# Optimization experiments

Measured on AMD Instinct MI355X. Metric: run time of the kernel, lower is better.

The kernel has to match this reference:

```python
import jax, jax.numpy as jnp
import numpy as np

D_MODEL = 1024
HEADS = 16
D_K = D_MODEL // HEADS
D_FF = 4096
EPS = 1e-6


def setup_inputs() -> dict:
    key = jax.random.key(0)
    ks = jax.random.split(key, 16)
    s = 1.0 / np.sqrt(D_MODEL)
    inp = {
        'x': jax.random.normal(ks[0], (4, 2048, D_MODEL), dtype=jnp.float32),
        'Wq': jax.random.normal(ks[1], (D_MODEL, D_MODEL), dtype=jnp.float32) * s,
        'bq': jnp.zeros((D_MODEL,), jnp.float32),
        'Wk': jax.random.normal(ks[2], (D_MODEL, D_MODEL), dtype=jnp.float32) * s,
        'bk': jnp.zeros((D_MODEL,), jnp.float32),
        'Wv': jax.random.normal(ks[3], (D_MODEL, D_MODEL), dtype=jnp.float32) * s,
        'bv': jnp.zeros((D_MODEL,), jnp.float32),
        'Wo': jax.random.normal(ks[4], (D_MODEL, D_MODEL), dtype=jnp.float32) * s,
        'bo': jnp.zeros((D_MODEL,), jnp.float32),
        'alpha1': jnp.ones((D_MODEL,), jnp.float32),
        'bias1': jnp.zeros((D_MODEL,), jnp.float32),
        'alpha2': jnp.ones((D_MODEL,), jnp.float32),
        'bias2': jnp.zeros((D_MODEL,), jnp.float32),
        'W1': jax.random.normal(ks[5], (D_MODEL, D_FF), dtype=jnp.float32) * s,
        'b1': jnp.zeros((D_FF,), jnp.float32),
        'W2': jax.random.normal(ks[6], (D_FF, D_MODEL), dtype=jnp.float32) * (1.0 / np.sqrt(D_FF)),
        'b2': jnp.zeros((D_MODEL,), jnp.float32),
    }
    return inp


def _residual_norm(x, residual, alpha, bias):
    # x = x + residual; norm with mean and UNBIASED std (torch x.std default),
    # eps added to std (not variance), affine alpha/bias. Dropout = identity (eval).
    s = x + residual
    mean = jnp.mean(s, axis=-1, keepdims=True)
    std = jnp.std(s, axis=-1, keepdims=True, ddof=1)
    return alpha * (s - mean) / (std + EPS) + bias


def _forward(x, Wq, bq, Wk, bk, Wv, bv, Wo, bo, alpha1, bias1, alpha2, bias2, W1, b1, W2, b2):
    B, S, D = x.shape
    # QKV projections and head split: (B, H, S, d_k)
    def split_heads(t):
        return t.reshape(B, S, HEADS, D_K).transpose(0, 2, 1, 3)
    Q = split_heads(x @ Wq + bq)
    K = split_heads(x @ Wk + bk)
    V = split_heads(x @ Wv + bv)
    # scaled dot-product attention (no mask, no dropout in eval)
    scores = jnp.einsum('bhqd,bhkd->bhqk', Q, K) / np.sqrt(D_K)
    weights = jax.nn.softmax(scores, axis=-1)
    attn = jnp.einsum('bhqk,bhkd->bhqd', weights, V)
    concat = attn.transpose(0, 2, 1, 3).reshape(B, S, D)
    attn_out = concat @ Wo + bo
    # post-norm residual 1
    norm1 = _residual_norm(attn_out, x, alpha1, bias1)
    # FFN (dropout = identity in eval)
    ff = jax.nn.relu(norm1 @ W1 + b1) @ W2 + b2
    # post-norm residual 2
    return _residual_norm(ff, norm1, alpha2, bias2)


def reference(x, Wq, bq, Wk, bk, Wv, bv, Wo, bo, alpha1, bias1, alpha2, bias2, W1, b1, W2, b2):
    return _forward(x, Wq, bq, Wk, bk, Wv, bv, Wo, bo, alpha1, bias1, alpha2, bias2, W1, b1, W2, b2)
```

## Files before the change

### kernel.cpp

```cpp
#include <hip/hip_runtime.h>
#include <hip/hip_bf16.h>
#include <stdint.h>

typedef __attribute__((ext_vector_type(8))) short bv8;
typedef __attribute__((ext_vector_type(4))) short sv4;
typedef __attribute__((ext_vector_type(4))) float f4;
typedef __attribute__((ext_vector_type(4))) unsigned uv4;

#define LDS_AS __attribute__((address_space(3)))
#define GLB_AS __attribute__((address_space(1)))

#if __has_builtin(__builtin_amdgcn_exp2f)
#define EXP2F(x) __builtin_amdgcn_exp2f(x)
#else
#define EXP2F(x) exp2f(x)
#endif

__device__ __forceinline__ void gload16(const void* g, void* l) {
  __builtin_amdgcn_global_load_lds((GLB_AS void*)(g), (LDS_AS void*)(l), 16, 0, 0);
}

__device__ __forceinline__ short f2bs(float x) {
  return __builtin_bit_cast(short, __float2bfloat16(x));
}
__device__ __forceinline__ float bs2f(short s) {
  unsigned u = ((unsigned)(unsigned short)s) << 16;
  return __builtin_bit_cast(float, u);
}
__device__ __forceinline__ unsigned cvtpk(float lo, float hi) {
  unsigned r;
  asm("v_cvt_pk_bf16_f32 %0, %1, %2" : "=v"(r) : "v"(lo), "v"(hi));
  return r;
}

__global__ __launch_bounds__(256) void k_cvt(const float* __restrict__ in, short* __restrict__ out) {
  const int i = (blockIdx.x * 256 + threadIdx.x) * 4;
  const float4 v = *(const float4*)(in + i);
  sv4 o; o[0] = f2bs(v.x); o[1] = f2bs(v.y); o[2] = f2bs(v.z); o[3] = f2bs(v.w);
  *(sv4*)(out + i) = o;
}

__global__ __launch_bounds__(256) void k_transpose(const float* __restrict__ W, short* __restrict__ Wt,
                                                   int K, int N) {
  __shared__ float tile[32][33];
  const int tx = threadIdx.x & 31, ty = threadIdx.x >> 5;
  const int n0 = blockIdx.x * 32, k0 = blockIdx.y * 32;
#pragma unroll
  for (int i = 0; i < 32; i += 8)
    tile[ty + i][tx] = W[(size_t)(k0 + ty + i) * N + n0 + tx];
  __syncthreads();
#pragma unroll
  for (int i = 0; i < 32; i += 8)
    Wt[(size_t)(n0 + ty + i) * K + k0 + tx] = f2bs(tile[tx][ty + i]);
}

template<int EPI>
__global__ __launch_bounds__(512) void k_gemm256(const short* __restrict__ A, const short* __restrict__ Bt,
                                                 const float* __restrict__ bias, const float* __restrict__ bias2,
                                                 const float* __restrict__ bias3,
                                                 short* __restrict__ C, short* __restrict__ D2,
                                                 short* __restrict__ D3,
                                                 int M, int N, int K, int nbx) {
  __shared__ __align__(16) short As[3][256 * 64];
  __shared__ __align__(16) short Bs[3][128 * 64];

  const int t = threadIdx.x;
  const int lane = t & 63, w = t >> 6;
  const int wm = w >> 1, wn = w & 1;
  const int lr = lane & 15, lg = lane >> 4;
  const int nwg = gridDim.x, cpx = nwg >> 3;
  const int bid = blockIdx.x;
  const int wid = (bid & 7) * cpx + (bid >> 3);
  const int by = wid / nbx, bx = wid % nbx;
  const int m0 = by * 256, n0 = bx * 128;
  const int nt = K >> 6;

  auto STAGE = [&](int k0, int bufi) {
    char* ad = (char*)As[bufi];
    char* bd = (char*)Bs[bufi];
#pragma unroll
    for (int i = 0; i < 4; ++i) {
      const int L = t * 16 + i * 8192;
      const int row = L >> 7;
      const int cbs = (L & 127) ^ ((row & 7) << 4);
      gload16(A + (size_t)(m0 + row) * K + k0 + (cbs >> 1), ad + L);
    }
#pragma unroll
    for (int i = 0; i < 2; ++i) {
      const int L = t * 16 + i * 8192;
      const int row = L >> 7;
      const int cbs = (L & 127) ^ ((row & 7) << 4);
      gload16(Bt + (size_t)(n0 + row) * K + k0 + (cbs >> 1), bd + L);
    }
  };

  f4 acc[4][4] = {};

  STAGE(0, 0);
  STAGE(64, 1);
  asm volatile("s_waitcnt vmcnt(6)" ::: "memory");
  __builtin_amdgcn_sched_barrier(0);
  __builtin_amdgcn_s_barrier();
  __builtin_amdgcn_sched_barrier(0);

  int cur = 0;
  for (int tt = 0; tt < nt; ++tt) {
    if (tt + 2 < nt) {
      int b2 = cur + 2; if (b2 >= 3) b2 -= 3;
      STAGE((tt + 2) << 6, b2);
    }
    const char* Ab = (const char*)As[cur];
    const char* Bb = (const char*)Bs[cur];
#pragma unroll
    for (int kk = 0; kk < 2; ++kk) {
      bv8 af[4], bf[4];
#pragma unroll
      for (int mi = 0; mi < 4; ++mi) {
        const int row = wm * 64 + mi * 16 + lr;
        const int cb = kk * 64 + lg * 16;
        af[mi] = *(const bv8*)(Ab + row * 128 + (cb ^ ((row & 7) << 4)));
      }
#pragma unroll
      for (int ni = 0; ni < 4; ++ni) {
        const int row = wn * 64 + ni * 16 + lr;
        const int cb = kk * 64 + lg * 16;
        bf[ni] = *(const bv8*)(Bb + row * 128 + (cb ^ ((row & 7) << 4)));
      }
      __builtin_amdgcn_s_setprio(1);
#pragma unroll
      for (int mi = 0; mi < 4; ++mi)
#pragma unroll
        for (int ni = 0; ni < 4; ++ni)
          acc[mi][ni] = __builtin_amdgcn_mfma_f32_16x16x32_bf16(af[mi], bf[ni], acc[mi][ni], 0, 0, 0);
      __builtin_amdgcn_s_setprio(0);
    }
    if (tt + 1 < nt) {
      if (tt + 2 < nt) asm volatile("s_waitcnt vmcnt(6)" ::: "memory");
      else             asm volatile("s_waitcnt vmcnt(0)" ::: "memory");
      __builtin_amdgcn_sched_barrier(0);
      __builtin_amdgcn_s_barrier();
      __builtin_amdgcn_sched_barrier(0);
    }
    cur += 1; if (cur >= 3) cur -= 3;
  }

#pragma unroll
  for (int ni = 0; ni < 4; ++ni) {
    const int c = n0 + wn * 64 + ni * 16 + lr;
    float bvs;
    int sel = 0, cc = c, h = 0, d = 0;
    if (EPI == 2) {
      sel = c >> 10; cc = c & 1023;
      bvs = (sel == 0 ? bias : sel == 1 ? bias2 : bias3)[cc];
      h = cc >> 6; d = cc & 63;
    } else {
      bvs = bias[c];
    }
#pragma unroll
    for (int mi = 0; mi < 4; ++mi) {
#pragma unroll
      for (int j = 0; j < 4; ++j) {
        const int r = m0 + wm * 64 + mi * 16 + lg * 4 + j;
        float v = acc[mi][ni][j] + bvs;
        if (EPI == 1) v = fmaxf(v, 0.f);
        if (EPI == 2) {
          const int bb = r >> 11, s = r & 2047;
          if (sel == 0)      C [((size_t)(bb * 16 + h) * 2048 + s) * 64 + d] = f2bs(v);
          else if (sel == 1) D2[((size_t)(bb * 16 + h) * 2048 + s) * 64 + d] = f2bs(v);
          else               D3[((size_t)(bb * 16 + h) * 64 + d) * 2048 + s] = f2bs(v);
        } else {
          C[(size_t)r * N + c] = f2bs(v);
        }
      }
    }
  }
}

__global__ __launch_bounds__(256) void k_attn(const short* __restrict__ Qg, const short* __restrict__ Kg,
                                              const short* __restrict__ Vtg, short* __restrict__ Oc) {
  __shared__ __align__(16) short Ks[2][128 * 64];

  const int t = threadIdx.x, lane = t & 63, w = t >> 6;
  const int lr = lane & 15, lg = lane >> 4;
  const int bid = blockIdx.x;
  const int wid = (bid & 7) * 128 + (bid >> 3);
  const int q0 = (wid & 15) * 128;
  const int bh = wid >> 4;
  const int b = bh >> 4, h = bh & 15;
  const short* Qp = Qg + (size_t)bh * 2048 * 64;
  const short* Kp = Kg + (size_t)bh * 2048 * 64;
  const short* Vp = Vtg + (size_t)bh * 64 * 2048;

  bv8 qf[2][2];
#pragma unroll
  for (int mi = 0; mi < 2; ++mi)
#pragma unroll
    for (int kk = 0; kk < 2; ++kk)
      qf[mi][kk] = *(const bv8*)(Qp + (size_t)(q0 + w * 32 + mi * 16 + lr) * 64 + kk * 32 + lg * 8);

  f4 Oa[2][4] = {};
  float lsum[2] = {0.f, 0.f};
  const float SC = 0.125f * 1.44269504089f;
  const bool hi = lg >= 2;
  const bool xx = (lg == 1) || (lg == 2);

#pragma unroll
  for (int i = 0; i < 4; ++i) {
    const int L = t * 16 + i * 4096;
    const int row = L >> 7;
    const int cbs = (L & 127) ^ ((row & 7) << 4);
    gload16(Kp + (size_t)row * 64 + (cbs >> 1), (char*)Ks[0] + L);
  }
  __syncthreads();

  int cur = 0;
  for (int kt = 0; kt < 2048; kt += 128) {
    if (kt + 128 < 2048) {
#pragma unroll
      for (int i = 0; i < 4; ++i) {
        const int L = t * 16 + i * 4096;
        const int row = L >> 7;
        const int cbs = (L & 127) ^ ((row & 7) << 4);
        gload16(Kp + (size_t)(kt + 128 + row) * 64 + (cbs >> 1), (char*)Ks[cur ^ 1] + L);
      }
    }
    const char* Kb = (const char*)Ks[cur];

#pragma unroll
    for (int hf = 0; hf < 2; ++hf) {
      f4 Sa[2][4] = {};
#pragma unroll
      for (int kk = 0; kk < 2; ++kk) {
        bv8 kf[4];
#pragma unroll
        for (int nl = 0; nl < 4; ++nl) {
          const int row = (hf * 4 + nl) * 16 + lr;
          const int cb = kk * 64 + lg * 16;
          kf[nl] = *(const bv8*)(Kb + row * 128 + (cb ^ ((row & 7) << 4)));
        }
        __builtin_amdgcn_s_setprio(1);
#pragma unroll
        for (int mi = 0; mi < 2; ++mi)
#pragma unroll
          for (int nl = 0; nl < 4; ++nl)
            Sa[mi][nl] = __builtin_amdgcn_mfma_f32_16x16x32_bf16(kf[nl], qf[mi][kk], Sa[mi][nl], 0, 0, 0);
        __builtin_amdgcn_s_setprio(0);
      }

#pragma unroll
      for (int mi = 0; mi < 2; ++mi) {
        float rs = 0.f;
#pragma unroll
        for (int nl = 0; nl < 4; ++nl)
#pragma unroll
          for (int j = 0; j < 4; ++j) {
            const float p = EXP2F(Sa[mi][nl][j] * SC);
            Sa[mi][nl][j] = p;
            rs += p;
          }
        lsum[mi] += rs;
      }

#pragma unroll
      for (int k2 = 0; k2 < 2; ++k2) {
        bv8 vf[4], pf[2];
#pragma unroll
        for (int nO = 0; nO < 4; ++nO)
          vf[nO] = *(const bv8*)(Vp + (size_t)(nO * 16 + lr) * 2048 + kt + hf * 64 + k2 * 32 + lg * 8);
#pragma unroll
        for (int mi = 0; mi < 2; ++mi) {
          const unsigned W0 = cvtpk(Sa[mi][2 * k2][0], Sa[mi][2 * k2][1]);
          const unsigned W1 = cvtpk(Sa[mi][2 * k2][2], Sa[mi][2 * k2][3]);
          const unsigned W2 = cvtpk(Sa[mi][2 * k2 + 1][0], Sa[mi][2 * k2 + 1][1]);
          const unsigned W3 = cvtpk(Sa[mi][2 * k2 + 1][2], Sa[mi][2 * k2 + 1][3]);
          const unsigned w0 = hi ? W2 : W0, w1 = hi ? W3 : W1;
          const unsigned s0 = __shfl_xor(hi ? W0 : W2, 32);
          const unsigned s1 = __shfl_xor(hi ? W1 : W3, 32);
          const unsigned t0 = __shfl_xor(xx ? w0 : s0, 16);
          const unsigned t1 = __shfl_xor(xx ? w1 : s1, 16);
          uv4 u;
          u[0] = (lg == 0) ? w0 : (lg == 2) ? s0 : t0;
          u[1] = (lg == 0) ? w1 : (lg == 2) ? s1 : t1;
          u[2] = (lg == 3) ? w0 : (lg == 1) ? s0 : t0;
          u[3] = (lg == 3) ? w1 : (lg == 1) ? s1 : t1;
          pf[mi] = __builtin_bit_cast(bv8, u);
        }
        __builtin_amdgcn_s_setprio(1);
#pragma unroll
        for (int mi = 0; mi < 2; ++mi)
#pragma unroll
          for (int nO = 0; nO < 4; ++nO)
            Oa[mi][nO] = __builtin_amdgcn_mfma_f32_16x16x32_bf16(vf[nO], pf[mi], Oa[mi][nO], 0, 0, 0);
        __builtin_amdgcn_s_setprio(0);
      }
    }

    __syncthreads();
    cur ^= 1;
  }

#pragma unroll
  for (int mi = 0; mi < 2; ++mi) {
    lsum[mi] += __shfl_xor(lsum[mi], 16);
    lsum[mi] += __shfl_xor(lsum[mi], 32);
  }

#pragma unroll
  for (int mi = 0; mi < 2; ++mi) {
    const float inv = 1.f / lsum[mi];
    const int q = q0 + w * 32 + mi * 16 + lr;
#pragma unroll
    for (int nO = 0; nO < 4; ++nO) {
      sv4 o;
#pragma unroll
      for (int j = 0; j < 4; ++j) o[j] = f2bs(Oa[mi][nO][j] * inv);
      const int c = h * 64 + nO * 16 + lg * 4;
      *(sv4*)(Oc + ((size_t)b * 2048 + q) * 1024 + c) = o;
    }
  }
}

template<int MODE>
__global__ __launch_bounds__(256) void k_resnorm(const short* __restrict__ a, const void* __restrict__ res,
                                                 const float* __restrict__ alpha, const float* __restrict__ beta,
                                                 void* __restrict__ out) {
  const int row = blockIdx.x;
  const int t = threadIdx.x;
  const int lane = t & 63, w = t >> 6;
  const size_t base = (size_t)row * 1024;

  const sv4 av = *(const sv4*)(a + base + t * 4);
  float v[4];
  if (MODE == 0) {
    const float4 rv = *(const float4*)((const float*)res + base + t * 4);
    v[0] = bs2f(av[0]) + rv.x; v[1] = bs2f(av[1]) + rv.y;
    v[2] = bs2f(av[2]) + rv.z; v[3] = bs2f(av[3]) + rv.w;
  } else {
    const sv4 rv = *(const sv4*)((const short*)res + base + t * 4);
#pragma unroll
    for (int i = 0; i < 4; ++i) v[i] = bs2f(av[i]) + bs2f(rv[i]);
  }
  float s = v[0] + v[1] + v[2] + v[3];
  float sq = v[0] * v[0] + v[1] * v[1] + v[2] * v[2] + v[3] * v[3];
#pragma unroll
  for (int m = 1; m < 64; m <<= 1) { s += __shfl_xor(s, m); sq += __shfl_xor(sq, m); }
  __shared__ float red[8];
  if (lane == 0) { red[w] = s; red[w + 4] = sq; }
  __syncthreads();
  s = red[0] + red[1] + red[2] + red[3];
  sq = red[4] + red[5] + red[6] + red[7];
  const float mean = s * (1.f / 1024.f);
  const float var = (sq - 1024.f * mean * mean) * (1.f / 1023.f);
  const float inv = 1.f / (sqrtf(fmaxf(var, 0.f)) + 1e-6f);
  const float4 al = *(const float4*)(alpha + t * 4);
  const float4 be = *(const float4*)(beta + t * 4);
  float y[4];
  y[0] = al.x * (v[0] - mean) * inv + be.x;
  y[1] = al.y * (v[1] - mean) * inv + be.y;
  y[2] = al.z * (v[2] - mean) * inv + be.z;
  y[3] = al.w * (v[3] - mean) * inv + be.w;
  if (MODE == 0) {
    sv4 o; o[0] = f2bs(y[0]); o[1] = f2bs(y[1]); o[2] = f2bs(y[2]); o[3] = f2bs(y[3]);
    *(sv4*)((short*)out + base + t * 4) = o;
  } else {
    *(float4*)((float*)out + base + t * 4) = make_float4(y[0], y[1], y[2], y[3]);
  }
}

extern "C" void kernel_launch(void* const* d_in, const int* in_sizes, int n_in,
                              void* d_out, int out_size, void* d_ws, size_t ws_size,
                              hipStream_t stream) {
  const float* x   = (const float*)d_in[0];
  const float* Wq  = (const float*)d_in[1];
  const float* bq  = (const float*)d_in[2];
  const float* Wk  = (const float*)d_in[3];
  const float* bk  = (const float*)d_in[4];
  const float* Wv  = (const float*)d_in[5];
  const float* bv  = (const float*)d_in[6];
  const float* Wo  = (const float*)d_in[7];
  const float* bo  = (const float*)d_in[8];
  const float* al1 = (const float*)d_in[9];
  const float* bi1 = (const float*)d_in[10];
  const float* al2 = (const float*)d_in[11];
  const float* bi2 = (const float*)d_in[12];
  const float* W1  = (const float*)d_in[13];
  const float* b1  = (const float*)d_in[14];
  const float* W2  = (const float*)d_in[15];
  const float* b2  = (const float*)d_in[16];

  if (ws_size < (size_t)136 * 1024 * 1024) return;

  char* ws = (char*)d_ws;
  short* xb  = (short*)(ws);
  short* Qb  = (short*)(ws + (16ll << 20));
  short* Kb  = (short*)(ws + (32ll << 20));
  short* Vtb = (short*)(ws + (48ll << 20));
  short* Hb  = (short*)(ws);
  short* Wqt = (short*)(ws + (64ll << 20));
  short* Wkt = (short*)(ws + (66ll << 20));
  short* Wvt = (short*)(ws + (68ll << 20));
  short* Wot = (short*)(ws + (70ll << 20));
  short* W1t = (short*)(ws + (72ll << 20));
  short* W2t = (short*)(ws + (80ll << 20));
  short* Cc  = (short*)(ws + (88ll << 20));
  short* AOb = (short*)(ws + (104ll << 20));
  short* N1b = (short*)(ws + (120ll << 20));
  short* FFb = (short*)(ws + (104ll << 20));

  k_cvt<<<8192, 256, 0, stream>>>(x, xb);
  k_transpose<<<dim3(32, 32), 256, 0, stream>>>(Wq, Wqt, 1024, 1024);
  k_transpose<<<dim3(32, 32), 256, 0, stream>>>(Wk, Wkt, 1024, 1024);
  k_transpose<<<dim3(32, 32), 256, 0, stream>>>(Wv, Wvt, 1024, 1024);
  k_transpose<<<dim3(32, 32), 256, 0, stream>>>(Wo, Wot, 1024, 1024);
  k_transpose<<<dim3(128, 32), 256, 0, stream>>>(W1, W1t, 1024, 4096);
  k_transpose<<<dim3(32, 128), 256, 0, stream>>>(W2, W2t, 4096, 1024);

  k_gemm256<2><<<768, 512, 0, stream>>>(xb, Wqt, bq, bk, bv, Qb, Kb, Vtb, 8192, 3072, 1024, 24);

  k_attn<<<1024, 256, 0, stream>>>(Qb, Kb, Vtb, Cc);

  k_gemm256<0><<<256, 512, 0, stream>>>(Cc, Wot, bo, nullptr, nullptr, AOb, nullptr, nullptr,
                                        8192, 1024, 1024, 8);
  k_resnorm<0><<<8192, 256, 0, stream>>>(AOb, x, al1, bi1, N1b);

  k_gemm256<1><<<1024, 512, 0, stream>>>(N1b, W1t, b1, nullptr, nullptr, Hb, nullptr, nullptr,
                                         8192, 4096, 1024, 32);
  k_gemm256<0><<<256, 512, 0, stream>>>(Hb, W2t, b2, nullptr, nullptr, FFb, nullptr, nullptr,
                                        8192, 1024, 4096, 8);
  k_resnorm<1><<<8192, 256, 0, stream>>>(FFb, N1b, al2, bi2, (float*)d_out);
}
```

Baseline: 505.4 us.

## Replace GEMM with 8-phase ping-pong schedule and wider N tiles

Replaces the triple-buffered 256x128 GEMM with a double-buffered kernel using 128x256 or 256x256 tiles. Each K step is split into four barrier-separated phases that interleave half-tile global-to-LDS loads, LDS fragment reads and MFMA blocks, in a ping-pong style. The aim is finer overlap of memory traffic with matrix math and more reuse from the wider tiles. The extra barriers add sync cost, and the larger accumulators raise register pressure.

```diff
diff --git a/kernel.cpp b/kernel.cpp
--- a/kernel.cpp
+++ b/kernel.cpp
@@ -16,6 +16,8 @@
 #define EXP2F(x) exp2f(x)
 #endif
 
+#define GBAR __builtin_amdgcn_s_barrier()
+
 __device__ __forceinline__ void gload16(const void* g, void* l) {
   __builtin_amdgcn_global_load_lds((GLB_AS void*)(g), (LDS_AS void*)(l), 16, 0, 0);
 }
@@ -54,113 +56,154 @@
     Wt[(size_t)(n0 + ty + i) * K + k0 + tx] = f2bs(tile[tx][ty + i]);
 }
 
-template<int EPI>
-__global__ __launch_bounds__(512) void k_gemm256(const short* __restrict__ A, const short* __restrict__ Bt,
-                                                 const float* __restrict__ bias, const float* __restrict__ bias2,
-                                                 const float* __restrict__ bias3,
-                                                 short* __restrict__ C, short* __restrict__ D2,
-                                                 short* __restrict__ D3,
-                                                 int M, int N, int K, int nbx) {
-  __shared__ __align__(16) short As[3][256 * 64];
-  __shared__ __align__(16) short Bs[3][128 * 64];
+template<int EPI, int MIH>
+__global__ __launch_bounds__(512) void k_gemm8p(
+    const short* __restrict__ A, const short* __restrict__ Bt,
+    const float* __restrict__ bias, const float* __restrict__ bias2, const float* __restrict__ bias3,
+    short* __restrict__ C, short* __restrict__ D2, short* __restrict__ D3,
+    int M, int N, int K, int nbx) {
+  constexpr int BM = MIH * 64;
+  constexpr int HOFF = (MIH == 4) ? 16384 : 4096;
+  __shared__ __align__(16) short SA[2][BM * 64];
+  __shared__ __align__(16) short SB[2][256 * 64];
 
   const int t = threadIdx.x;
   const int lane = t & 63, w = t >> 6;
-  const int wm = w >> 1, wn = w & 1;
+  const int wr = w >> 2, wc = w & 3;
   const int lr = lane & 15, lg = lane >> 4;
-  const int nwg = gridDim.x, cpx = nwg >> 3;
+  const int cpx = gridDim.x >> 3;
   const int bid = blockIdx.x;
   const int wid = (bid & 7) * cpx + (bid >> 3);
   const int by = wid / nbx, bx = wid % nbx;
-  const int m0 = by * 256, n0 = bx * 128;
+  const int m0 = by * BM, n0 = bx * 256;
   const int nt = K >> 6;
-
-  auto STAGE = [&](int k0, int bufi) {
-    char* ad = (char*)As[bufi];
-    char* bd = (char*)Bs[bufi];
-#pragma unroll
-    for (int i = 0; i < 4; ++i) {
-      const int L = t * 16 + i * 8192;
-      const int row = L >> 7;
-      const int cbs = (L & 127) ^ ((row & 7) << 4);
-      gload16(A + (size_t)(m0 + row) * K + k0 + (cbs >> 1), ad + L);
-    }
+  const int swz = ((t >> 3) & 7) << 4;
+  const int rbyte0 = (lg * 16) ^ ((lr & 7) << 4);
+  const int rbyte1 = (64 + lg * 16) ^ ((lr & 7) << 4);
+
+  auto ST_A = [&](int k0, int half, int buf) {
 #pragma unroll
     for (int i = 0; i < 2; ++i) {
       const int L = t * 16 + i * 8192;
-      const int row = L >> 7;
-      const int cbs = (L & 127) ^ ((row & 7) << 4);
-      gload16(Bt + (size_t)(n0 + row) * K + k0 + (cbs >> 1), bd + L);
+      const int cbs = (L & 127) ^ swz;
+      const int grow = (MIH == 4) ? (m0 + i * 128 + half * 64 + (t >> 3))
+                                  : (m0 + i * 64 + (t >> 3));
+      gload16(A + (size_t)grow * K + k0 + (cbs >> 1),
+              (char*)SA[buf] + (MIH == 4 ? half * 16384 : 0) + L);
     }
   };
-
-  f4 acc[4][4] = {};
-
-  STAGE(0, 0);
-  STAGE(64, 1);
-  asm volatile("s_waitcnt vmcnt(6)" ::: "memory");
-  __builtin_amdgcn_sched_barrier(0);
-  __builtin_amdgcn_s_barrier();
-  __builtin_amdgcn_sched_barrier(0);
-
-  int cur = 0;
-  for (int tt = 0; tt < nt; ++tt) {
-    if (tt + 2 < nt) {
-      int b2 = cur + 2; if (b2 >= 3) b2 -= 3;
-      STAGE((tt + 2) << 6, b2);
-    }
-    const char* Ab = (const char*)As[cur];
-    const char* Bb = (const char*)Bs[cur];
-#pragma unroll
-    for (int kk = 0; kk < 2; ++kk) {
-      bv8 af[4], bf[4];
-#pragma unroll
-      for (int mi = 0; mi < 4; ++mi) {
-        const int row = wm * 64 + mi * 16 + lr;
-        const int cb = kk * 64 + lg * 16;
-        af[mi] = *(const bv8*)(Ab + row * 128 + (cb ^ ((row & 7) << 4)));
-      }
-#pragma unroll
-      for (int ni = 0; ni < 4; ++ni) {
-        const int row = wn * 64 + ni * 16 + lr;
-        const int cb = kk * 64 + lg * 16;
-        bf[ni] = *(const bv8*)(Bb + row * 128 + (cb ^ ((row & 7) << 4)));
-      }
-      __builtin_amdgcn_s_setprio(1);
-#pragma unroll
-      for (int mi = 0; mi < 4; ++mi)
-#pragma unroll
-        for (int ni = 0; ni < 4; ++ni)
-          acc[mi][ni] = __builtin_amdgcn_mfma_f32_16x16x32_bf16(af[mi], bf[ni], acc[mi][ni], 0, 0, 0);
-      __builtin_amdgcn_s_setprio(0);
-    }
-    if (tt + 1 < nt) {
-      if (tt + 2 < nt) asm volatile("s_waitcnt vmcnt(6)" ::: "memory");
-      else             asm volatile("s_waitcnt vmcnt(0)" ::: "memory");
-      __builtin_amdgcn_sched_barrier(0);
-      __builtin_amdgcn_s_barrier();
-      __builtin_amdgcn_sched_barrier(0);
-    }
-    cur += 1; if (cur >= 3) cur -= 3;
+  auto ST_B = [&](int k0, int half, int buf) {
+#pragma unroll
+    for (int i = 0; i < 2; ++i) {
+      const int L = t * 16 + i * 8192;
+      const int rr = (t >> 3) + i * 64;
+      const int cbs = (L & 127) ^ swz;
+      const int grow = n0 + (rr >> 5) * 64 + half * 32 + (rr & 31);
+      gload16(Bt + (size_t)grow * K + k0 + (cbs >> 1),
+              (char*)SB[buf] + half * 16384 + L);
+    }
+  };
+
+  f4 acc[2 * MIH][4] = {};
+  bv8 af[MIH][2], bflo[2][2], bfhi[2][2];
+
+  auto LDA = [&](int buf, int half) {
+    const char* base = (const char*)SA[buf] + half * HOFF + wr * 8192;
+#pragma unroll
+    for (int m = 0; m < MIH; ++m) {
+      af[m][0] = *(const bv8*)(base + (m * 16 + lr) * 128 + rbyte0);
+      af[m][1] = *(const bv8*)(base + (m * 16 + lr) * 128 + rbyte1);
+    }
+  };
+  auto LDB = [&](int buf, int half, bv8 (&bf)[2][2]) {
+    const char* base = (const char*)SB[buf] + half * 16384 + wc * 4096;
+#pragma unroll
+    for (int n = 0; n < 2; ++n) {
+      bf[n][0] = *(const bv8*)(base + (n * 16 + lr) * 128 + rbyte0);
+      bf[n][1] = *(const bv8*)(base + (n * 16 + lr) * 128 + rbyte1);
+    }
+  };
+  auto MM = [&](bv8 (&bf)[2][2], int mB, int nB) {
+    __builtin_amdgcn_s_setprio(1);
+#pragma unroll
+    for (int kk = 0; kk < 2; ++kk)
+#pragma unroll
+      for (int m = 0; m < MIH; ++m)
+#pragma unroll
+        for (int n = 0; n < 2; ++n)
+          acc[mB + m][nB + n] = __builtin_amdgcn_mfma_f32_16x16x32_bf16(
+              af[m][kk], bf[n][kk], acc[mB + m][nB + n], 0, 0, 0);
+    __builtin_amdgcn_s_setprio(0);
+  };
+
+  ST_A(0, 0, 0); if (MIH == 4) ST_A(0, 1, 0);
+  ST_B(0, 0, 0); ST_B(0, 1, 0);
+  ST_A(64, 0, 1);
+  ST_B(64, 1, 1);
+  if (MIH == 4) { ST_A(64, 1, 1); asm volatile("s_waitcnt vmcnt(6)" ::: "memory"); }
+  else          { asm volatile("s_waitcnt vmcnt(4)" ::: "memory"); }
+  GBAR;
+
+  const int nIter = nt >> 1;
+  for (int it = 0; it < nIter; ++it) {
+    const int k1 = (2 * it + 1) << 6;
+    const int k2 = (2 * it + 2) << 6, k3 = (2 * it + 3) << 6;
+    const bool h2 = (2 * it + 2) < nt, h3 = (2 * it + 3) < nt;
+
+    LDA(0, 0); LDB(0, 0, bflo);
+    ST_B(k1, 0, 1);
+    GBAR; MM(bflo, 0, 0); GBAR;
+    LDB(0, 1, bfhi);
+    if (h2 && MIH == 4) ST_A(k2, 0, 0);
+    GBAR; MM(bfhi, 0, 2); GBAR;
+    LDA(0, 1);
+    if (h2) ST_B(k2, 1, 0);
+    GBAR; MM(bfhi, MIH, 2); GBAR;
+    if (h2) ST_A(k2, (MIH == 4) ? 1 : 0, 0);
+    if (h2) {
+      if (MIH == 4) asm volatile("s_waitcnt vmcnt(6)" ::: "memory");
+      else          asm volatile("s_waitcnt vmcnt(4)" ::: "memory");
+    } else {
+      asm volatile("s_waitcnt vmcnt(0)" ::: "memory");
+    }
+    GBAR; MM(bflo, MIH, 0); GBAR;
+
+    LDA(1, 0); LDB(1, 0, bflo);
+    if (h2) ST_B(k2, 0, 0);
+    GBAR; MM(bflo, 0, 0); GBAR;
+    LDB(1, 1, bfhi);
+    if (h3 && MIH == 4) ST_A(k3, 0, 1);
+    GBAR; MM(bfhi, 0, 2); GBAR;
+    LDA(1, 1);
+    if (h3) ST_B(k3, 1, 1);
+    GBAR; MM(bfhi, MIH, 2); GBAR;
+    if (h3) ST_A(k3, (MIH == 4) ? 1 : 0, 1);
+    if (h3) {
+      if (MIH == 4) asm volatile("s_waitcnt vmcnt(6)" ::: "memory");
+      else          asm volatile("s_waitcnt vmcnt(4)" ::: "memory");
+    } else {
+      asm volatile("s_waitcnt vmcnt(0)" ::: "memory");
+    }
+    GBAR; MM(bflo, MIH, 0); GBAR;
   }
 
 #pragma unroll
   for (int ni = 0; ni < 4; ++ni) {
-    const int c = n0 + wn * 64 + ni * 16 + lr;
+    const int c = n0 + wc * 64 + ni * 16 + lr;
     float bvs;
-    int sel = 0, cc = c, h = 0, d = 0;
+    int sel = 0, h = 0, d = 0;
     if (EPI == 2) {
-      sel = c >> 10; cc = c & 1023;
+      sel = c >> 10; const int cc = c & 1023;
       bvs = (sel == 0 ? bias : sel == 1 ? bias2 : bias3)[cc];
       h = cc >> 6; d = cc & 63;
     } else {
       bvs = bias[c];
     }
 #pragma unroll
-    for (int mi = 0; mi < 4; ++mi) {
+    for (int mi = 0; mi < 2 * MIH; ++mi) {
 #pragma unroll
       for (int j = 0; j < 4; ++j) {
-        const int r = m0 + wm * 64 + mi * 16 + lg * 4 + j;
+        const int r = m0 + wr * (MIH * 32) + mi * 16 + lg * 4 + j;
         float v = acc[mi][ni][j] + bvs;
         if (EPI == 1) v = fmaxf(v, 0.f);
         if (EPI == 2) {
@@ -415,17 +458,17 @@
   k_transpose<<<dim3(128, 32), 256, 0, stream>>>(W1, W1t, 1024, 4096);
   k_transpose<<<dim3(32, 128), 256, 0, stream>>>(W2, W2t, 4096, 1024);
 
-  k_gemm256<2><<<768, 512, 0, stream>>>(xb, Wqt, bq, bk, bv, Qb, Kb, Vtb, 8192, 3072, 1024, 24);
+  k_gemm8p<2, 2><<<768, 512, 0, stream>>>(xb, Wqt, bq, bk, bv, Qb, Kb, Vtb, 8192, 3072, 1024, 12);
 
   k_attn<<<1024, 256, 0, stream>>>(Qb, Kb, Vtb, Cc);
 
-  k_gemm256<0><<<256, 512, 0, stream>>>(Cc, Wot, bo, nullptr, nullptr, AOb, nullptr, nullptr,
-                                        8192, 1024, 1024, 8);
+  k_gemm8p<0, 2><<<256, 512, 0, stream>>>(Cc, Wot, bo, nullptr, nullptr, AOb, nullptr, nullptr,
+                                          8192, 1024, 1024, 4);
   k_resnorm<0><<<8192, 256, 0, stream>>>(AOb, x, al1, bi1, N1b);
 
-  k_gemm256<1><<<1024, 512, 0, stream>>>(N1b, W1t, b1, nullptr, nullptr, Hb, nullptr, nullptr,
-                                         8192, 4096, 1024, 32);
-  k_gemm256<0><<<256, 512, 0, stream>>>(Hb, W2t, b2, nullptr, nullptr, FFb, nullptr, nullptr,
-                                        8192, 1024, 4096, 8);
+  k_gemm8p<1, 4><<<512, 512, 0, stream>>>(N1b, W1t, b1, nullptr, nullptr, Hb, nullptr, nullptr,
+                                          8192, 4096, 1024, 16);
+  k_gemm8p<0, 2><<<256, 512, 0, stream>>>(Hb, W2t, b2, nullptr, nullptr, FFb, nullptr, nullptr,
+                                          8192, 1024, 4096, 4);
   k_resnorm<1><<<8192, 256, 0, stream>>>(FFb, N1b, al2, bi2, (float*)d_out);
 }
```

Result: faster. 473.9 us (-6.2%).
